# Kernel tuning notes

Measured on AMD Instinct MI355X. Metric: run time of the kernel, lower is better.

## Reference

```python
import jax, jax.numpy as jnp
from jax import lax
import numpy as np

OBJECT_W, BCE_W, DICE_W = 2.0, 5.0, 5.0
B, N, M, C = 8, 128, 32, 65536


def setup_inputs() -> dict:
    key = jax.random.key(0)
    k1, k2, k3 = jax.random.split(key, 3)
    objectness = jax.random.normal(k1, (B, N), jnp.float32)
    pred_masks = jax.random.normal(k2, (B, N, C), jnp.float32)
    gt_masks = jax.random.randint(k3, (B, M, C), 0, 2).astype(jnp.float32)
    return {"objectness": objectness, "pred_masks": pred_masks, "gt_masks": gt_masks}


def _cost_matrices(objectness, pred, gt):
    # BCE-with-logits vs all-ones target: log(1+exp(-x)) = softplus(-x)
    # BCE-with-logits vs all-zeros target: softplus(x)
    sp_pos = jax.nn.softplus(-pred)                       # [B,N,C]
    sp_neg = jax.nn.softplus(pred)                        # [B,N,C]
    # einsum('nc,mc->nm', pos, t) + einsum('nc,mc->nm', neg, 1-t), batched.
    # neg @ (1-t) = neg.sum(c) - neg @ t (avoids materializing 1-t).
    bce = (jnp.einsum('bnc,bmc->bnm', sp_pos, gt)
           + sp_neg.sum(-1)[:, :, None]
           - jnp.einsum('bnc,bmc->bnm', sp_neg, gt)) / pred.shape[-1]
    s = jax.nn.sigmoid(pred)
    numerator = 2.0 * jnp.einsum('bnc,bmc->bnm', s, gt)
    denominator = s.sum(-1)[:, :, None] + gt.sum(-1)[:, None, :]
    dice = 1.0 - (numerator + 1.0) / (denominator + 1.0)
    obj = -jax.nn.sigmoid(objectness)[:, :, None]         # [B,N,1]
    return OBJECT_W * obj + BCE_W * bce + DICE_W * dice    # [B,N,M]


def _lsap(cost):
    """Jonker-Volgenant shortest-augmenting-path LSAP (scipy algorithm).
    cost: [R, C] with R <= C. Returns col4row [R] int32: column per row."""
    R, Cn = cost.shape
    BIG = jnp.float32(1e30)

    def outer(cur_row, carry):
        u, v, row4col, col4row = carry
        shortest = jnp.full((Cn,), BIG, jnp.float32)
        path = jnp.full((Cn,), -1, jnp.int32)
        SR = jnp.zeros((R,), bool)
        SC = jnp.zeros((Cn,), bool)

        def sp_cond(s):
            return s[6] < 0

        def sp_body(s):
            i, shortest, path, SR, SC, minVal, sink = s
            SR = SR.at[i].set(True)
            d = minVal + cost[i] - u[i] - v
            better = (d < shortest) & (~SC)
            shortest = jnp.where(better, d, shortest)
            path = jnp.where(better, i, path)
            masked = jnp.where(SC, BIG, shortest)
            j = jnp.argmin(masked).astype(jnp.int32)
            minVal = masked[j]
            SC = SC.at[j].set(True)
            nxt = row4col[j]
            sink = jnp.where(nxt == -1, j, jnp.int32(-1))
            i = jnp.where(nxt == -1, i, nxt)
            return (i, shortest, path, SR, SC, minVal, sink)

        init = (cur_row.astype(jnp.int32), shortest, path, SR, SC,
                jnp.float32(0.0), jnp.int32(-1))
        i, shortest, path, SR, SC, minVal, sink = lax.while_loop(sp_cond, sp_body, init)

        # dual updates (scipy rectangular_lsap)
        u = u.at[cur_row].add(minVal)
        extra = SR & (jnp.arange(R) != cur_row)
        sp_at_col = shortest[jnp.clip(col4row, 0, Cn - 1)]
        u = jnp.where(extra, u + minVal - sp_at_col, u)
        v = jnp.where(SC, v - (minVal - shortest), v)

        # augment along path
        def aug_cond(s):
            return ~s[3]

        def aug_body(s):
            j, row4col, col4row, done = s
            i = path[j]
            row4col = row4col.at[j].set(i)
            tmp = col4row[i]
            col4row = col4row.at[i].set(j)
            done = (i == cur_row)
            return (tmp, row4col, col4row, done)

        _, row4col, col4row, _ = lax.while_loop(
            aug_cond, aug_body, (sink, row4col, col4row, jnp.array(False)))
        return (u, v, row4col, col4row)

    carry = (jnp.zeros((R,), jnp.float32), jnp.zeros((Cn,), jnp.float32),
             jnp.full((Cn,), -1, jnp.int32), jnp.full((R,), -1, jnp.int32))
    u, v, row4col, col4row = lax.fori_loop(0, R, outer, carry)
    return col4row


def reference(objectness, pred_masks, gt_masks):
    cost = _cost_matrices(objectness, pred_masks, gt_masks)   # [B,N,M]
    # scipy lsap on [N,M] then sort by target == solving on cost.T [M,N]:
    # indices[b, m] = matched query index for target m.
    indices = jax.vmap(_lsap)(jnp.transpose(cost, (0, 2, 1)))  # [B,M]
    return cost, indices
```

## Files before the change

kernel.cpp:

```cpp
#include <hip/hip_runtime.h>
#include <hip/hip_bf16.h>

#define LOG2E 1.4426950408889634f
#define LN2   0.6931471805599453f

typedef __attribute__((ext_vector_type(8))) short short8;
typedef __attribute__((ext_vector_type(4))) float f32x4;

#define B_ 8
#define N_ 128
#define M_ 32
#define C_ 65536
#define KCHUNKS 64
#define KC (C_ / KCHUNKS)
#define BK 64
#define AST 72

__device__ __forceinline__ unsigned pack2(float lo, float hi) {
  union { __hip_bfloat16 h; unsigned short s; } a, b;
  a.h = __float2bfloat16(lo);
  b.h = __float2bfloat16(hi);
  return (unsigned)a.s | ((unsigned)b.s << 16);
}

__global__ __launch_bounds__(256, 2) void cost_partial_kernel(
    const float* __restrict__ pred, const float* __restrict__ gt,
    float* __restrict__ xg_part, float* __restrict__ sg_part,
    float* __restrict__ sp_part, float* __restrict__ ss_part,
    float* __restrict__ gts_part)
{
  __shared__ unsigned short As[256 * AST];
  __shared__ unsigned short Bt[32 * AST];
  const int kc = blockIdx.x, b = blockIdx.y;
  const int tid = threadIdx.x;
  const int grp = tid >> 4, gl = tid & 15;
  const int grow = tid >> 3, gh = tid & 7;
  const int wave = tid >> 6, lane = tid & 63;
  const int quad = lane >> 4, lcol = lane & 15;
  const int c0 = kc * KC;
  const int slab = kc * B_ + b;

  const float* predB = pred + (size_t)b * N_ * C_ + c0;
  const float* gtB   = gt   + (size_t)b * M_ * C_ + (size_t)grow * C_ + c0;

  float spr[8], sr[8], gtacc = 0.f;
#pragma unroll
  for (int r = 0; r < 8; ++r) { spr[r] = 0.f; sr[r] = 0.f; }

  f32x4 acc[4][2];
#pragma unroll
  for (int rt = 0; rt < 4; ++rt)
#pragma unroll
    for (int ct = 0; ct < 2; ++ct)
      acc[rt][ct] = (f32x4){0.f, 0.f, 0.f, 0.f};

  float4 p[8], g0, g1;
#pragma unroll
  for (int r = 0; r < 8; ++r)
    p[r] = *(const float4*)(predB + (size_t)(r * 16 + grp) * C_ + gl * 4);
  g0 = *(const float4*)(gtB + gh * 4);
  g1 = *(const float4*)(gtB + (gh + 8) * 4);

  for (int ks = 0; ks < KC / BK; ++ks) {
    float4 pn[8], gn0, gn1;
    if (ks + 1 < KC / BK) {
      const int cb = (ks + 1) * BK;
#pragma unroll
      for (int r = 0; r < 8; ++r)
        pn[r] = *(const float4*)(predB + (size_t)(r * 16 + grp) * C_ + cb + gl * 4);
      gn0 = *(const float4*)(gtB + cb + gh * 4);
      gn1 = *(const float4*)(gtB + cb + (gh + 8) * 4);
    }

#pragma unroll
    for (int r = 0; r < 8; ++r) {
      const int row = r * 16 + grp;
      float xs[4] = {p[r].x, p[r].y, p[r].z, p[r].w};
      float ss[4];
#pragma unroll
      for (int e = 0; e < 4; ++e) {
        float x = xs[e];
        float t = fminf(x * LOG2E, 80.f);
        float e2 = __builtin_amdgcn_exp2f(t);
        float z = 1.f + e2;
        float s = e2 * __builtin_amdgcn_rcpf(z);
        spr[r] += __builtin_amdgcn_logf(z);
        sr[r]  += s;
        ss[e] = s;
      }
      *(uint2*)&As[row * AST + gl * 4] =
          (uint2){pack2(xs[0], xs[1]), pack2(xs[2], xs[3])};
      *(uint2*)&As[(N_ + row) * AST + gl * 4] =
          (uint2){pack2(ss[0], ss[1]), pack2(ss[2], ss[3])};
    }
    gtacc += g0.x + g0.y + g0.z + g0.w + g1.x + g1.y + g1.z + g1.w;
    *(uint2*)&Bt[grow * AST + gh * 4] =
        (uint2){pack2(g0.x, g0.y), pack2(g0.z, g0.w)};
    *(uint2*)&Bt[grow * AST + (gh + 8) * 4] =
        (uint2){pack2(g1.x, g1.y), pack2(g1.z, g1.w)};
    __syncthreads();

#pragma unroll
    for (int k0 = 0; k0 < BK; k0 += 32) {
      const int koff = k0 + quad * 8;
      short8 bf0 = *(const short8*)&Bt[lcol * AST + koff];
      short8 bf1 = *(const short8*)&Bt[(16 + lcol) * AST + koff];
#pragma unroll
      for (int rt = 0; rt < 4; ++rt) {
        short8 af = *(const short8*)&As[(wave * 64 + rt * 16 + lcol) * AST + koff];
        acc[rt][0] = __builtin_amdgcn_mfma_f32_16x16x32_bf16(af, bf0, acc[rt][0], 0, 0, 0);
        acc[rt][1] = __builtin_amdgcn_mfma_f32_16x16x32_bf16(af, bf1, acc[rt][1], 0, 0, 0);
      }
    }
    __syncthreads();

    if (ks + 1 < KC / BK) {
#pragma unroll
      for (int r = 0; r < 8; ++r) p[r] = pn[r];
      g0 = gn0; g1 = gn1;
    }
  }

#pragma unroll
  for (int r = 0; r < 8; ++r) {
    float v1 = spr[r], v2 = sr[r];
#pragma unroll
    for (int off = 1; off < 16; off <<= 1) {
      v1 += __shfl_xor(v1, off);
      v2 += __shfl_xor(v2, off);
    }
    if (gl == 0) {
      sp_part[slab * N_ + r * 16 + grp] = v1 * LN2;
      ss_part[slab * N_ + r * 16 + grp] = v2;
    }
  }
  gtacc += __shfl_xor(gtacc, 1);
  gtacc += __shfl_xor(gtacc, 2);
  gtacc += __shfl_xor(gtacc, 4);
  if (gh == 0) gts_part[slab * M_ + grow] = gtacc;

#pragma unroll
  for (int rt = 0; rt < 4; ++rt)
#pragma unroll
    for (int ct = 0; ct < 2; ++ct)
#pragma unroll
      for (int reg = 0; reg < 4; ++reg) {
        int orow = wave * 64 + rt * 16 + quad * 4 + reg;
        int ocol = ct * 16 + lcol;
        float v = acc[rt][ct][reg];
        if (orow < N_) xg_part[(slab * N_ + orow) * M_ + ocol] = v;
        else           sg_part[(slab * N_ + (orow - N_)) * M_ + ocol] = v;
      }
}

__global__ void finalize_kernel(const float* __restrict__ obj,
    const float* __restrict__ xg_part, const float* __restrict__ sg_part,
    const float* __restrict__ sp_part, const float* __restrict__ ss_part,
    const float* __restrict__ gts_part, float* __restrict__ cost)
{
  int idx = blockIdx.x * blockDim.x + threadIdx.x;
  int b = idx >> 12;
  int n = (idx >> 5) & 127;
  int m = idx & 31;
  float xa = 0.f, sa = 0.f, spa = 0.f, ssa = 0.f, ga = 0.f;
#pragma unroll 4
  for (int kc = 0; kc < KCHUNKS; ++kc) {
    int slab = kc * B_ + b;
    xa  += xg_part[(slab * N_ + n) * M_ + m];
    sa  += sg_part[(slab * N_ + n) * M_ + m];
    spa += sp_part[slab * N_ + n];
    ssa += ss_part[slab * N_ + n];
    ga  += gts_part[slab * M_ + m];
  }
  float o = obj[b * N_ + n];
  float t = fminf(o * LOG2E, 80.f);
  float e2 = __builtin_amdgcn_exp2f(t);
  float sig = e2 * __builtin_amdgcn_rcpf(1.f + e2);
  float bce = (spa - xa) * (1.0f / (float)C_);
  float dice = 1.f - (2.f * sa + 1.f) / (ssa + ga + 1.f);
  cost[idx] = -2.f * sig + 5.f * bce + 5.f * dice;
}

#define BIGF 1e30f

__device__ __forceinline__ float wave_min_all(float x) {
  const int BI = __builtin_bit_cast(int, BIGF);
  int v = __builtin_bit_cast(int, x);
#define MIN_STEP(ctrl)                                                        \
  {                                                                           \
    int t_ = __builtin_amdgcn_update_dpp(BI, v, ctrl, 0xf, 0xf, false);       \
    v = __builtin_bit_cast(int, fminf(__builtin_bit_cast(float, v),           \
                                      __builtin_bit_cast(float, t_)));        \
  }
  MIN_STEP(0x111)
  MIN_STEP(0x112)
  MIN_STEP(0x114)
  MIN_STEP(0x118)
  MIN_STEP(0x142)
  MIN_STEP(0x143)
#undef MIN_STEP
  return __builtin_bit_cast(float, __builtin_amdgcn_readlane(v, 63));
}

__device__ __forceinline__ float rdlane_f(float x, int l) {
  return __builtin_bit_cast(float, __builtin_amdgcn_readlane(__builtin_bit_cast(int, x), l));
}

__global__ __launch_bounds__(64) void lsap_kernel(const float* __restrict__ cost,
                                                  float* __restrict__ out)
{
  const int b = blockIdx.x;
  const int lane = threadIdx.x;
  __shared__ float cTs[M_ * 129];

#pragma unroll 4
  for (int t = 0; t < 16; ++t) {
    int e = t * 256 + lane * 4;
    float4 v4 = *(const float4*)&cost[b * 4096 + e];
    int n = e >> 5, m = e & 31;
    cTs[(m + 0) * 129 + n] = v4.x;
    cTs[(m + 1) * 129 + n] = v4.y;
    cTs[(m + 2) * 129 + n] = v4.z;
    cTs[(m + 3) * 129 + n] = v4.w;
  }
  __syncthreads();

  float u_reg = 0.f;
  int c4r = -1;
  float v0 = 0.f, v1 = 0.f;
  int r40 = -1, r41 = -1;

  for (int cur = 0; cur < M_; ++cur) {
    float sh0 = BIGF, sh1 = BIGF;
    int p0 = -1, p1 = -1;
    bool sc0 = false, sc1 = false;
    unsigned srmask = 0u;
    int i = cur, sink = -1;
    float minVal = 0.f;

    while (sink < 0) {
      srmask |= 1u << i;
      float ui = rdlane_f(u_reg, i);
      float cc0 = cTs[i * 129 + 2 * lane];
      float cc1 = cTs[i * 129 + 2 * lane + 1];
      float d0 = ((minVal + cc0) - ui) - v0;
      float d1 = ((minVal + cc1) - ui) - v1;
      if (!sc0 && d0 < sh0) { sh0 = d0; p0 = i; }
      if (!sc1 && d1 < sh1) { sh1 = d1; p1 = i; }
      float m0 = sc0 ? BIGF : sh0;
      float m1 = sc1 ? BIGF : sh1;
      float mv = wave_min_all(fminf(m0, m1));
      unsigned long long bl0 = __ballot(m0 == mv);
      unsigned long long bl1 = __ballot(m1 == mv);
      int j0 = bl0 ? 2 * (int)__builtin_ctzll(bl0) : 0x7fffffff;
      int j1 = bl1 ? 2 * (int)__builtin_ctzll(bl1) + 1 : 0x7fffffff;
      int j = j0 < j1 ? j0 : j1;
      minVal = mv;
      if (lane == (j >> 1)) { if (j & 1) sc1 = true; else sc0 = true; }
      int nxt = __builtin_amdgcn_readlane((j & 1) ? r41 : r40, j >> 1);
      if (nxt < 0) sink = j; else i = nxt;
    }

    int jj = c4r < 0 ? 0 : c4r;
    float g0 = __shfl(sh0, jj >> 1);
    float g1 = __shfl(sh1, jj >> 1);
    float sj = (jj & 1) ? g1 : g0;
    if (lane < M_) {
      if (lane == cur) u_reg += minVal;
      else if ((srmask >> lane) & 1u) u_reg += minVal - sj;
    }
    if (sc0) v0 -= minVal - sh0;
    if (sc1) v1 -= minVal - sh1;

    int j = sink;
    while (true) {
      int i2 = __builtin_amdgcn_readlane((j & 1) ? p1 : p0, j >> 1);
      if (lane == (j >> 1)) { if (j & 1) r41 = i2; else r40 = i2; }
      int tmp = __builtin_amdgcn_readlane(c4r, i2);
      if (lane == i2) c4r = j;
      if (i2 == cur) break;
      j = tmp;
    }
  }
  if (lane < M_) out[b * M_ + lane] = (float)c4r;
}

extern "C" void kernel_launch(void* const* d_in, const int* in_sizes, int n_in,
                              void* d_out, int out_size, void* d_ws, size_t ws_size,
                              hipStream_t stream)
{
  const float* obj  = (const float*)d_in[0];
  const float* pred = (const float*)d_in[1];
  const float* gt   = (const float*)d_in[2];
  float* out = (float*)d_out;

  float* xg_part  = (float*)d_ws;
  float* sg_part  = xg_part + (size_t)KCHUNKS * B_ * N_ * M_;
  float* sp_part  = sg_part + (size_t)KCHUNKS * B_ * N_ * M_;
  float* ss_part  = sp_part + (size_t)KCHUNKS * B_ * N_;
  float* gts_part = ss_part + (size_t)KCHUNKS * B_ * N_;

  cost_partial_kernel<<<dim3(KCHUNKS, B_), 256, 0, stream>>>(
      pred, gt, xg_part, sg_part, sp_part, ss_part, gts_part);
  finalize_kernel<<<dim3(32768 / 64), 64, 0, stream>>>(
      obj, xg_part, sg_part, sp_part, ss_part, gts_part, out);
  lsap_kernel<<<dim3(B_), 64, 0, stream>>>(out, out + 32768);
}
```

Before: 571.2 us.

## Drop register prefetch, merge softplus logs into one product log, retune finalize

The explicit register double-buffering of pred/gt loads is removed, so each step now loads its own tile directly. Four log calls per row group become one log of a product of (1+e^x) terms, and the exp clamps are dropped in both kernels. The finalize kernel now launches 128-thread blocks. Dropping the prefetch may expose global load latency. Without the clamp, large logits or a product of four large terms can overflow to inf, so the softplus sum becomes fragile.

```diff
diff --git a/kernel.cpp b/kernel.cpp
--- a/kernel.cpp
+++ b/kernel.cpp
@@ -54,40 +54,31 @@
     for (int ct = 0; ct < 2; ++ct)
       acc[rt][ct] = (f32x4){0.f, 0.f, 0.f, 0.f};
 
-  float4 p[8], g0, g1;
-#pragma unroll
-  for (int r = 0; r < 8; ++r)
-    p[r] = *(const float4*)(predB + (size_t)(r * 16 + grp) * C_ + gl * 4);
-  g0 = *(const float4*)(gtB + gh * 4);
-  g1 = *(const float4*)(gtB + (gh + 8) * 4);
-
   for (int ks = 0; ks < KC / BK; ++ks) {
-    float4 pn[8], gn0, gn1;
-    if (ks + 1 < KC / BK) {
-      const int cb = (ks + 1) * BK;
-#pragma unroll
-      for (int r = 0; r < 8; ++r)
-        pn[r] = *(const float4*)(predB + (size_t)(r * 16 + grp) * C_ + cb + gl * 4);
-      gn0 = *(const float4*)(gtB + cb + gh * 4);
-      gn1 = *(const float4*)(gtB + cb + (gh + 8) * 4);
-    }
+    const int cb = ks * BK;
+    float4 p[8];
+#pragma unroll
+    for (int r = 0; r < 8; ++r)
+      p[r] = *(const float4*)(predB + (size_t)(r * 16 + grp) * C_ + cb + gl * 4);
+    float4 g0 = *(const float4*)(gtB + cb + gh * 4);
+    float4 g1 = *(const float4*)(gtB + cb + (gh + 8) * 4);
 
 #pragma unroll
     for (int r = 0; r < 8; ++r) {
       const int row = r * 16 + grp;
       float xs[4] = {p[r].x, p[r].y, p[r].z, p[r].w};
       float ss[4];
+      float prod = 1.f;
 #pragma unroll
       for (int e = 0; e < 4; ++e) {
-        float x = xs[e];
-        float t = fminf(x * LOG2E, 80.f);
-        float e2 = __builtin_amdgcn_exp2f(t);
+        float e2 = __builtin_amdgcn_exp2f(xs[e] * LOG2E);
         float z = 1.f + e2;
         float s = e2 * __builtin_amdgcn_rcpf(z);
-        spr[r] += __builtin_amdgcn_logf(z);
-        sr[r]  += s;
+        prod *= z;
+        sr[r] += s;
         ss[e] = s;
       }
+      spr[r] += __builtin_amdgcn_logf(prod);
       *(uint2*)&As[row * AST + gl * 4] =
           (uint2){pack2(xs[0], xs[1]), pack2(xs[2], xs[3])};
       *(uint2*)&As[(N_ + row) * AST + gl * 4] =
@@ -113,12 +104,6 @@
       }
     }
     __syncthreads();
-
-    if (ks + 1 < KC / BK) {
-#pragma unroll
-      for (int r = 0; r < 8; ++r) p[r] = pn[r];
-      g0 = gn0; g1 = gn1;
-    }
   }
 
 #pragma unroll
@@ -173,8 +158,7 @@
     ga  += gts_part[slab * M_ + m];
   }
   float o = obj[b * N_ + n];
-  float t = fminf(o * LOG2E, 80.f);
-  float e2 = __builtin_amdgcn_exp2f(t);
+  float e2 = __builtin_amdgcn_exp2f(o * LOG2E);
   float sig = e2 * __builtin_amdgcn_rcpf(1.f + e2);
   float bce = (spa - xa) * (1.0f / (float)C_);
   float dice = 1.f - (2.f * sa + 1.f) / (ssa + ga + 1.f);
@@ -302,7 +286,7 @@
 
   cost_partial_kernel<<<dim3(KCHUNKS, B_), 256, 0, stream>>>(
       pred, gt, xg_part, sg_part, sp_part, ss_part, gts_part);
-  finalize_kernel<<<dim3(32768 / 64), 64, 0, stream>>>(
+  finalize_kernel<<<dim3(32768 / 128), 128, 0, stream>>>(
       obj, xg_part, sg_part, sp_part, ss_part, gts_part, out);
   lsap_kernel<<<dim3(B_), 64, 0, stream>>>(out, out + 32768);
 }
```

Measured after the change: 571.3 us. No clear change (+0.0%).
